# Performance work log

Measured on AMD Instinct MI355X. Metric: run time of the kernel, lower is better.

Reference implementation:

```python
import jax, jax.numpy as jnp
import numpy as np

N_HEADS = 8
OUT_FEATURES = 64
LEAKY_SLOPE = 0.2
MASK_FILL = -1e9


def setup_inputs() -> dict:
    key = jax.random.key(0)
    k_h, k_adj, k_W, k_a = jax.random.split(key, 4)
    B, N, F_IN = 1, 4096, 128
    h = jax.random.normal(k_h, (B, N, F_IN), dtype=jnp.float32)
    adj_mat = jax.random.randint(k_adj, (N, N), 0, 2, dtype=jnp.int32)
    # glorot-style scaled params
    W = jax.random.normal(k_W, (F_IN, OUT_FEATURES * N_HEADS), dtype=jnp.float32) * (1.0 / np.sqrt(F_IN))
    a = jax.random.normal(k_a, (N_HEADS, 2 * OUT_FEATURES, 1), dtype=jnp.float32) * (1.0 / np.sqrt(2 * OUT_FEATURES))
    return {"h": h, "adj_mat": adj_mat, "W": W, "a": a}


def reference(h, adj_mat, W, a):
    B, N, _ = h.shape
    heads = a.shape[0]
    out = a.shape[1] // 2
    # linear transform + head split (same reshape order as tf.reshape)
    ht = jnp.reshape(h @ W, (-1, heads, N, out))            # (B, heads, N, out)
    # additive attention scores
    src = jnp.einsum('bhnf,hfo->bhno', ht, a[:, :out, :])    # (B, heads, N, 1)
    tgt = jnp.einsum('bhnf,hfo->bhno', ht, a[:, out:, :])    # (B, heads, N, 1)
    e = src + jnp.swapaxes(tgt, -1, -2)                      # (B, heads, N, N)
    e = jnp.where(e > 0, e, LEAKY_SLOPE * e)                 # leaky_relu
    e = jnp.where(adj_mat > 0, e, MASK_FILL)                 # adjacency mask
    attention = jax.nn.softmax(e, axis=-1)
    h_prime = attention @ ht                                 # (B, heads, N, out)
    return h_prime
```

## Files before the change

### kernel.cpp

```cpp
#include <hip/hip_runtime.h>
#include <stdint.h>

#define HT_STRIDE 262144
#define LOG2E 1.4426950408889634f

typedef __attribute__((ext_vector_type(8))) short bf16x8;
typedef __attribute__((ext_vector_type(4))) float f32x4;

__device__ __forceinline__ unsigned short f2bf(float f) {
    unsigned int u = __float_as_uint(f);
    u += 0x7FFFu + ((u >> 16) & 1u);
    return (unsigned short)(u >> 16);
}

__device__ __forceinline__ float exp2_fast(float e) {
#if __has_builtin(__builtin_amdgcn_exp2f)
    return __builtin_amdgcn_exp2f(e);
#else
    return __expf(e * 0.6931471805599453f);
#endif
}

__global__ void __launch_bounds__(256) k_fused(const float* __restrict__ h,
                                               const int* __restrict__ adj,
                                               const float* __restrict__ W,
                                               const float* __restrict__ aW,
                                               float* __restrict__ src,
                                               float* __restrict__ tgt,
                                               unsigned short* __restrict__ htT2,
                                               unsigned int* __restrict__ abm) {
    __shared__ unsigned int ldsT[1024];
    __shared__ float hs[8][128];
    __shared__ float ldsA[64][66];
    __shared__ float redS[4][64];
    __shared__ float redT[4][64];
    const int t = threadIdx.x;

    if (blockIdx.x < 512) {
        const int lane = t & 63;
        const int w = t >> 6;
        const int sb = blockIdx.x >> 3;
        const int cq = blockIdx.x & 7;
        for (int rr = 0; rr < 16; ++rr) {
            const int* arow = adj + (sb * 64 + w * 16 + rr) * 4096 + cq * 512;
            int v[8];
            #pragma unroll
            for (int j = 0; j < 8; ++j) v[j] = arow[j * 64 + lane];
            #pragma unroll
            for (int j = 0; j < 8; ++j) {
                unsigned long long m = __ballot(v[j] > 0);
                if (lane < 2)
                    ldsT[(2 * j + lane) * 64 + rr * 4 + w] = (unsigned int)(m >> (lane * 32));
            }
        }
        __syncthreads();
        ((uint4*)(abm + (sb * 128 + cq * 16) * 64))[t] = ((uint4*)ldsT)[t];
    } else {
        const int bid2 = (int)blockIdx.x - 512;
        const int n0 = bid2 * 8;
        const int p0 = bid2 * 64;
        const int hd = p0 >> 12;
        const int m0 = p0 & 4095;

        {
            float4 v = ((const float4*)(h + n0 * 128))[t];
            int e = t * 4;
            int r = e >> 7, f = e & 127;
            hs[r][f + 0] = v.x; hs[r][f + 1] = v.y;
            hs[r][f + 2] = v.z; hs[r][f + 3] = v.w;
        }
        __syncthreads();

        float acc0[8], acc1[8];
        #pragma unroll
        for (int r = 0; r < 8; ++r) { acc0[r] = 0.f; acc1[r] = 0.f; }
        const float2* Wf = (const float2*)W;
        for (int f = 0; f < 128; ++f) {
            float2 wp = Wf[f * 256 + t];
            #pragma unroll
            for (int r = 0; r < 8; ++r) {
                float hv = hs[r][f];
                acc0[r] = fmaf(hv, wp.x, acc0[r]);
                acc1[r] = fmaf(hv, wp.y, acc1[r]);
            }
        }
        {
            const int ns = t >> 5;
            const int o = (2 * t) & 63;
            #pragma unroll
            for (int r = 0; r < 8; ++r) {
                *(float2*)&ldsA[r * 8 + ns][o] = make_float2(acc0[r], acc1[r]);
            }
        }
        __syncthreads();

        {
            const int r = t & 63, og = t >> 6;
            float sdot = 0.f, gdot = 0.f;
            #pragma unroll
            for (int k = 0; k < 16; ++k) {
                int o = og * 16 + k;
                float hv = ldsA[r][o];
                sdot = fmaf(hv, aW[hd * 128 + o], sdot);
                gdot = fmaf(hv, aW[hd * 128 + 64 + o], gdot);
            }
            redS[og][r] = sdot; redT[og][r] = gdot;
        }
        __syncthreads();
        if (t < 64) {
            src[p0 + t] = (redS[0][t] + redS[1][t] + redS[2][t] + redS[3][t]) * LOG2E;
        } else if (t < 128) {
            int r = t - 64;
            tgt[p0 + r] = (redT[0][r] + redT[1][r] + redT[2][r] + redT[3][r]) * LOG2E;
        }

        unsigned short* d = htT2 + (hd * 128 + (m0 >> 5)) * 2048;
        #pragma unroll
        for (int i = 0; i < 16; ++i) {
            int id = t + 256 * i;
            int mi = id & 31, o = (id >> 5) & 63, ct = id >> 11;
            d[ct * 2048 + o * 32 + mi] = f2bf(ldsA[mi + 32 * ct][o]);
        }
    }
}

__global__ void __launch_bounds__(256, 4) k_attn(const unsigned int* __restrict__ abm,
                                                 const unsigned short* __restrict__ htT2,
                                                 const float* __restrict__ srcv,
                                                 const float* __restrict__ tgtv,
                                                 float* __restrict__ out) {
    __shared__ __align__(16) float smem[6912];
    uint2* bm2 = (uint2*)smem;

    const int t = threadIdx.x;
    const int kq = t >> 6;
    const int lane = t & 63;
    const int li = lane & 15;
    const int quad = lane >> 4;
    const int head = blockIdx.x & 7;
    const int s32 = blockIdx.x >> 3;
    const int s64 = s32 >> 1, half = s32 & 1;
    const int i0 = s32 * 32;

    {
        const unsigned int* base = abm + s64 * 8192 + half * 2;
        #pragma unroll
        for (int i = 0; i < 8; ++i) {
            int p = t + 256 * i;
            int c = p >> 4, lw = p & 15;
            bm2[p] = *(const uint2*)(base + c * 64 + lw * 4);
        }
    }

    float a_[2], b_[2];
    #pragma unroll
    for (int g2 = 0; g2 < 2; ++g2) {
        float sv = srcv[head * 4096 + i0 + 16 * g2 + li];
        a_[g2] = sv;
        b_[g2] = 0.2f * sv;
    }

    f32x4 acc[8];
    #pragma unroll
    for (int i = 0; i < 8; ++i) acc[i] = (f32x4){0.f, 0.f, 0.f, 0.f};
    float pd[2] = {0.f, 0.f};

    const float4* tgtp = (const float4*)(tgtv + head * 4096);
    const uint4*  ap   = (const uint4*)(htT2 + head * HT_STRIDE) + (li * 4 + quad);

    __syncthreads();

    const int c0 = kq * 32;
    #pragma unroll 1
    for (int ci = 0; ci < 32; ++ci) {
        const int c = c0 + ci;
        uint4 av0 = ap[c * 256 + 0];
        uint4 av1 = ap[c * 256 + 64];
        uint4 av2 = ap[c * 256 + 128];
        uint4 av3 = ap[c * 256 + 192];
        float4 tg0 = tgtp[c * 8 + quad * 2 + 0];
        float4 tg1 = tgtp[c * 8 + quad * 2 + 1];
        uint2 bw = bm2[c * 16 + li];

        const float tt[8] = {tg0.x, tg0.y, tg0.z, tg0.w, tg1.x, tg1.y, tg1.z, tg1.w};
        const unsigned int wb[2] = {bw.x, bw.y};
        #pragma unroll
        for (int g2 = 0; g2 < 2; ++g2) {
            const unsigned int wq = wb[g2] >> (quad * 8);
            float wv[8];
            #pragma unroll
            for (int j = 0; j < 8; ++j) {
                float t1 = tt[j] + a_[g2];
                float t2 = fmaf(tt[j], 0.2f, b_[g2]);
                float e = fmaxf(t1, t2);
                float p = exp2_fast(e);
                wv[j] = (wq & (1u << j)) ? p : 0.f;
                pd[g2] += wv[j];
            }
            unsigned int pk0, pk1, pk2, pk3;
            asm("v_cvt_pk_bf16_f32 %0, %1, %2" : "=v"(pk0) : "v"(wv[0]), "v"(wv[1]));
            asm("v_cvt_pk_bf16_f32 %0, %1, %2" : "=v"(pk1) : "v"(wv[2]), "v"(wv[3]));
            asm("v_cvt_pk_bf16_f32 %0, %1, %2" : "=v"(pk2) : "v"(wv[4]), "v"(wv[5]));
            asm("v_cvt_pk_bf16_f32 %0, %1, %2" : "=v"(pk3) : "v"(wv[6]), "v"(wv[7]));
            uint4 bv; bv.x = pk0; bv.y = pk1; bv.z = pk2; bv.w = pk3;
            bf16x8 bfrag = __builtin_bit_cast(bf16x8, bv);
            acc[g2 * 4 + 0] = __builtin_amdgcn_mfma_f32_16x16x32_bf16(__builtin_bit_cast(bf16x8, av0), bfrag, acc[g2 * 4 + 0], 0, 0, 0);
            acc[g2 * 4 + 1] = __builtin_amdgcn_mfma_f32_16x16x32_bf16(__builtin_bit_cast(bf16x8, av1), bfrag, acc[g2 * 4 + 1], 0, 0, 0);
            acc[g2 * 4 + 2] = __builtin_amdgcn_mfma_f32_16x16x32_bf16(__builtin_bit_cast(bf16x8, av2), bfrag, acc[g2 * 4 + 2], 0, 0, 0);
            acc[g2 * 4 + 3] = __builtin_amdgcn_mfma_f32_16x16x32_bf16(__builtin_bit_cast(bf16x8, av3), bfrag, acc[g2 * 4 + 3], 0, 0, 0);
        }
    }

    __syncthreads();
    if (kq != 0) {
        float* cb = smem + ((kq - 1) * 64 + lane) * 36;
        #pragma unroll
        for (int i = 0; i < 8; ++i) ((f32x4*)cb)[i] = acc[i];
        cb[32] = pd[0]; cb[33] = pd[1];
    }
    __syncthreads();
    if (kq == 0) {
        #pragma unroll
        for (int q = 0; q < 3; ++q) {
            const float* cb = smem + (q * 64 + lane) * 36;
            #pragma unroll
            for (int i = 0; i < 8; ++i) acc[i] += ((const f32x4*)cb)[i];
            pd[0] += cb[32]; pd[1] += cb[33];
        }
        #pragma unroll
        for (int g2 = 0; g2 < 2; ++g2) {
            float p2 = pd[g2];
            p2 += __shfl_xor(p2, 16, 64);
            p2 += __shfl_xor(p2, 32, 64);
            const float rd = 1.0f / p2;
            float4* op = (float4*)(out + head * HT_STRIDE + (i0 + 16 * g2 + li) * 64);
            #pragma unroll
            for (int f = 0; f < 4; ++f) {
                f32x4 a = acc[g2 * 4 + f];
                op[f * 4 + quad] = make_float4(a[0] * rd, a[1] * rd, a[2] * rd, a[3] * rd);
            }
        }
    }
}

extern "C" void kernel_launch(void* const* d_in, const int* in_sizes, int n_in,
                              void* d_out, int out_size, void* d_ws, size_t ws_size,
                              hipStream_t stream) {
    const float* h   = (const float*)d_in[0];
    const int*   adj = (const int*)d_in[1];
    const float* W   = (const float*)d_in[2];
    const float* aW  = (const float*)d_in[3];
    float* out = (float*)d_out;

    char* ws = (char*)d_ws;
    float* src  = (float*)(ws);
    float* tgt  = (float*)(ws + 131072);
    unsigned int*   abm  = (unsigned int*)(ws + 262144);
    unsigned short* htT2 = (unsigned short*)(ws + 2359296);

    hipLaunchKernelGGL(k_fused, dim3(1024), dim3(256), 0, stream,
                       h, adj, W, aW, src, tgt, htT2, abm);
    hipLaunchKernelGGL(k_attn,  dim3(1024), dim3(256), 0, stream,
                       abm, htT2, src, tgt, out);
}
```

Measured before the change: 156.8 us.

## Prefetch value tiles, stage tgt in LDS, compute row sums via MFMA

The attention kernel now double-buffers the bf16 value fragments for the next key chunk in registers so global loads overlap the current chunk's compute. The per-head tgt vector is copied into shared memory once per block instead of being read from global memory each iteration. The softmax denominator is accumulated by an extra MFMA against a ones matrix on the bf16-rounded weights, which replaces the scalar adds and cross-lane shuffles. Packed f32x2 arithmetic is used for the leaky-relu terms. The cost is more registers and LDS per block, which may reduce occupancy, and the denominator now sums bf16-rounded weights.

```diff
diff --git a/kernel.cpp b/kernel.cpp
--- a/kernel.cpp
+++ b/kernel.cpp
@@ -6,6 +6,7 @@
 
 typedef __attribute__((ext_vector_type(8))) short bf16x8;
 typedef __attribute__((ext_vector_type(4))) float f32x4;
+typedef __attribute__((ext_vector_type(2))) float f32x2;
 
 __device__ __forceinline__ unsigned short f2bf(float f) {
     unsigned int u = __float_as_uint(f);
@@ -129,8 +130,9 @@
                                                  const float* __restrict__ srcv,
                                                  const float* __restrict__ tgtv,
                                                  float* __restrict__ out) {
-    __shared__ __align__(16) float smem[6912];
-    uint2* bm2 = (uint2*)smem;
+    __shared__ __align__(16) float smem[8192];
+    float* tgl = smem;
+    uint2* bm2 = (uint2*)(smem + 4096);
 
     const int t = threadIdx.x;
     const int kq = t >> 6;
@@ -143,6 +145,11 @@
     const int i0 = s32 * 32;
 
     {
+        const float4* tsrc = (const float4*)(tgtv + head * 4096);
+        float4* tdst = (float4*)tgl;
+        #pragma unroll
+        for (int i = 0; i < 4; ++i) tdst[t + 256 * i] = tsrc[t + 256 * i];
+
         const unsigned int* base = abm + s64 * 8192 + half * 2;
         #pragma unroll
         for (int i = 0; i < 8; ++i) {
@@ -152,34 +159,44 @@
         }
     }
 
-    float a_[2], b_[2];
+    f32x2 a2[2], b2[2];
     #pragma unroll
     for (int g2 = 0; g2 < 2; ++g2) {
         float sv = srcv[head * 4096 + i0 + 16 * g2 + li];
-        a_[g2] = sv;
-        b_[g2] = 0.2f * sv;
+        a2[g2] = (f32x2){sv, sv};
+        b2[g2] = (f32x2){0.2f * sv, 0.2f * sv};
     }
 
     f32x4 acc[8];
     #pragma unroll
     for (int i = 0; i < 8; ++i) acc[i] = (f32x4){0.f, 0.f, 0.f, 0.f};
-    float pd[2] = {0.f, 0.f};
-
-    const float4* tgtp = (const float4*)(tgtv + head * 4096);
-    const uint4*  ap   = (const uint4*)(htT2 + head * HT_STRIDE) + (li * 4 + quad);
+    f32x4 apd[2];
+    apd[0] = (f32x4){0.f, 0.f, 0.f, 0.f};
+    apd[1] = (f32x4){0.f, 0.f, 0.f, 0.f};
+
+    const uint4 onesw = {0x3F803F80u, 0x3F803F80u, 0x3F803F80u, 0x3F803F80u};
+    const bf16x8 aones = __builtin_bit_cast(bf16x8, onesw);
+
+    const uint4* ap = (const uint4*)(htT2 + head * HT_STRIDE) + (li * 4 + quad);
 
     __syncthreads();
 
     const int c0 = kq * 32;
-    #pragma unroll 1
+    uint4 avb[2][4];
+    #pragma unroll
+    for (int f = 0; f < 4; ++f) avb[0][f] = ap[c0 * 256 + f * 64];
+
+    #pragma unroll 2
     for (int ci = 0; ci < 32; ++ci) {
+        const int cur = ci & 1;
         const int c = c0 + ci;
-        uint4 av0 = ap[c * 256 + 0];
-        uint4 av1 = ap[c * 256 + 64];
-        uint4 av2 = ap[c * 256 + 128];
-        uint4 av3 = ap[c * 256 + 192];
-        float4 tg0 = tgtp[c * 8 + quad * 2 + 0];
-        float4 tg1 = tgtp[c * 8 + quad * 2 + 1];
+        const int cn = c0 + ((ci + 1) & 31);
+        #pragma unroll
+        for (int f = 0; f < 4; ++f) avb[cur ^ 1][f] = ap[cn * 256 + f * 64];
+
+        const float* tk = tgl + c * 32 + quad * 8;
+        float4 tg0 = ((const float4*)tk)[0];
+        float4 tg1 = ((const float4*)tk)[1];
         uint2 bw = bm2[c * 16 + li];
 
         const float tt[8] = {tg0.x, tg0.y, tg0.z, tg0.w, tg1.x, tg1.y, tg1.z, tg1.w};
@@ -187,27 +204,25 @@
         #pragma unroll
         for (int g2 = 0; g2 < 2; ++g2) {
             const unsigned int wq = wb[g2] >> (quad * 8);
-            float wv[8];
-            #pragma unroll
-            for (int j = 0; j < 8; ++j) {
-                float t1 = tt[j] + a_[g2];
-                float t2 = fmaf(tt[j], 0.2f, b_[g2]);
-                float e = fmaxf(t1, t2);
-                float p = exp2_fast(e);
-                wv[j] = (wq & (1u << j)) ? p : 0.f;
-                pd[g2] += wv[j];
-            }
-            unsigned int pk0, pk1, pk2, pk3;
-            asm("v_cvt_pk_bf16_f32 %0, %1, %2" : "=v"(pk0) : "v"(wv[0]), "v"(wv[1]));
-            asm("v_cvt_pk_bf16_f32 %0, %1, %2" : "=v"(pk1) : "v"(wv[2]), "v"(wv[3]));
-            asm("v_cvt_pk_bf16_f32 %0, %1, %2" : "=v"(pk2) : "v"(wv[4]), "v"(wv[5]));
-            asm("v_cvt_pk_bf16_f32 %0, %1, %2" : "=v"(pk3) : "v"(wv[6]), "v"(wv[7]));
-            uint4 bv; bv.x = pk0; bv.y = pk1; bv.z = pk2; bv.w = pk3;
+            unsigned int pk[4];
+            #pragma unroll
+            for (int m = 0; m < 4; ++m) {
+                f32x2 tp = (f32x2){tt[2 * m], tt[2 * m + 1]};
+                f32x2 t1 = tp + a2[g2];
+                f32x2 t2 = tp * 0.2f + b2[g2];
+                float p0e = exp2_fast(fmaxf(t1[0], t2[0]));
+                float p1e = exp2_fast(fmaxf(t1[1], t2[1]));
+                float w0 = (wq & (1u << (2 * m)))     ? p0e : 0.f;
+                float w1 = (wq & (1u << (2 * m + 1))) ? p1e : 0.f;
+                asm("v_cvt_pk_bf16_f32 %0, %1, %2" : "=v"(pk[m]) : "v"(w0), "v"(w1));
+            }
+            uint4 bv; bv.x = pk[0]; bv.y = pk[1]; bv.z = pk[2]; bv.w = pk[3];
             bf16x8 bfrag = __builtin_bit_cast(bf16x8, bv);
-            acc[g2 * 4 + 0] = __builtin_amdgcn_mfma_f32_16x16x32_bf16(__builtin_bit_cast(bf16x8, av0), bfrag, acc[g2 * 4 + 0], 0, 0, 0);
-            acc[g2 * 4 + 1] = __builtin_amdgcn_mfma_f32_16x16x32_bf16(__builtin_bit_cast(bf16x8, av1), bfrag, acc[g2 * 4 + 1], 0, 0, 0);
-            acc[g2 * 4 + 2] = __builtin_amdgcn_mfma_f32_16x16x32_bf16(__builtin_bit_cast(bf16x8, av2), bfrag, acc[g2 * 4 + 2], 0, 0, 0);
-            acc[g2 * 4 + 3] = __builtin_amdgcn_mfma_f32_16x16x32_bf16(__builtin_bit_cast(bf16x8, av3), bfrag, acc[g2 * 4 + 3], 0, 0, 0);
+            apd[g2] = __builtin_amdgcn_mfma_f32_16x16x32_bf16(aones, bfrag, apd[g2], 0, 0, 0);
+            acc[g2 * 4 + 0] = __builtin_amdgcn_mfma_f32_16x16x32_bf16(__builtin_bit_cast(bf16x8, avb[cur][0]), bfrag, acc[g2 * 4 + 0], 0, 0, 0);
+            acc[g2 * 4 + 1] = __builtin_amdgcn_mfma_f32_16x16x32_bf16(__builtin_bit_cast(bf16x8, avb[cur][1]), bfrag, acc[g2 * 4 + 1], 0, 0, 0);
+            acc[g2 * 4 + 2] = __builtin_amdgcn_mfma_f32_16x16x32_bf16(__builtin_bit_cast(bf16x8, avb[cur][2]), bfrag, acc[g2 * 4 + 2], 0, 0, 0);
+            acc[g2 * 4 + 3] = __builtin_amdgcn_mfma_f32_16x16x32_bf16(__builtin_bit_cast(bf16x8, avb[cur][3]), bfrag, acc[g2 * 4 + 3], 0, 0, 0);
         }
     }
 
@@ -216,10 +231,11 @@
         float* cb = smem + ((kq - 1) * 64 + lane) * 36;
         #pragma unroll
         for (int i = 0; i < 8; ++i) ((f32x4*)cb)[i] = acc[i];
-        cb[32] = pd[0]; cb[33] = pd[1];
+        cb[32] = apd[0][0]; cb[33] = apd[1][0];
     }
     __syncthreads();
     if (kq == 0) {
+        float pd[2] = {apd[0][0], apd[1][0]};
         #pragma unroll
         for (int q = 0; q < 3; ++q) {
             const float* cb = smem + (q * 64 + lane) * 36;
@@ -229,10 +245,7 @@
         }
         #pragma unroll
         for (int g2 = 0; g2 < 2; ++g2) {
-            float p2 = pd[g2];
-            p2 += __shfl_xor(p2, 16, 64);
-            p2 += __shfl_xor(p2, 32, 64);
-            const float rd = 1.0f / p2;
+            const float rd = 1.0f / pd[g2];
             float4* op = (float4*)(out + head * HT_STRIDE + (i0 + 16 * g2 + li) * 64);
             #pragma unroll
             for (int f = 0; f < 4; ++f) {
```

New measurement: 155.5 us. About the same (-0.9%).
